# Performance work log

Measured on AMD Instinct MI355X. Metric: run time of the kernel, lower is better.

## Reference

```python
import jax, jax.numpy as jnp
import numpy as np

B_GRAPHS = 256
N_PER = 512
N = B_GRAPHS * N_PER            # 131072 nodes
E = 1048576                     # edges (avg degree 8)
H = 64                          # hidden_dim
L = 3                           # num_layers
R = 128                         # rnn_dim
NODE_IN = 2
EDGE_IN = 2
OUT = 2
JK = L * H


def setup_inputs() -> dict:
    key = jax.random.key(0)
    ks = jax.random.split(key, 40)
    # intra-graph random edges
    g = jax.random.randint(ks[0], (E,), 0, B_GRAPHS)
    src = g * N_PER + jax.random.randint(ks[1], (E,), 0, N_PER)
    dst = g * N_PER + jax.random.randint(ks[2], (E,), 0, N_PER)
    edge_index = jnp.stack([src, dst]).astype(jnp.int64)
    batch = jnp.repeat(jnp.arange(B_GRAPHS, dtype=jnp.int64), N_PER)

    p = lambda k, shp: jax.random.normal(k, shp, jnp.float32) * 0.1
    return dict(
        x=jax.random.normal(ks[3], (N, NODE_IN), jnp.float32),
        edge_attr=jax.random.normal(ks[4], (E, EDGE_IN), jnp.float32),
        node_W=p(ks[5], (NODE_IN, H)), node_b=p(ks[6], (H,)),
        edgeemb_W=p(ks[7], (EDGE_IN, H)), edgeemb_b=p(ks[8], (H,)),
        gat_W=p(ks[9], (L, H, H)), gat_Wedge=p(ks[10], (L, H, H)),
        gat_att_src=p(ks[11], (L, H)), gat_att_dst=p(ks[12], (L, H)),
        gat_att_edge=p(ks[13], (L, H)), gat_b=p(ks[14], (L, H)),
        gru_wih_f=p(ks[15], (3 * R, JK)), gru_whh_f=p(ks[16], (3 * R, R)),
        gru_bih_f=p(ks[17], (3 * R,)), gru_bhh_f=p(ks[18], (3 * R,)),
        gru_wih_b=p(ks[19], (3 * R, JK)), gru_whh_b=p(ks[20], (3 * R, R)),
        gru_bih_b=p(ks[21], (3 * R,)), gru_bhh_b=p(ks[22], (3 * R,)),
        head_W1=p(ks[23], (2 * R, 64)), head_b1=p(ks[24], (64,)),
        head_W2=p(ks[25], (64, OUT)), head_b2=p(ks[26], (OUT,)),
        edge_index=edge_index, batch=batch,
    )


def _gru_dir(xs, wih, whh, bih, bhh):
    # xs: [T, B, F] -> outputs [T, B, R]  (PyTorch GRU cell equations)
    gx = xs @ wih.T + bih  # precompute input gates [T, B, 3R]
    h0 = jnp.zeros((xs.shape[1], R), xs.dtype)

    def step(h, g):
        gh = h @ whh.T + bhh
        r = jax.nn.sigmoid(g[..., :R] + gh[..., :R])
        z = jax.nn.sigmoid(g[..., R:2 * R] + gh[..., R:2 * R])
        n = jnp.tanh(g[..., 2 * R:] + r * gh[..., 2 * R:])
        hn = (1.0 - z) * n + z * h
        return hn, hn

    _, ys = jax.lax.scan(step, h0, gx)
    return ys


def _forward(x, edge_attr, node_W, node_b, edgeemb_W, edgeemb_b,
             gat_W, gat_Wedge, gat_att_src, gat_att_dst, gat_att_edge, gat_b,
             gru_wih_f, gru_whh_f, gru_bih_f, gru_bhh_f,
             gru_wih_b, gru_whh_b, gru_bih_b, gru_bhh_b,
             head_W1, head_b1, head_W2, head_b2, edge_index, batch):
    src, dst = edge_index[0], edge_index[1]
    h = x @ node_W + node_b                     # [N, H]
    e = edge_attr @ edgeemb_W + edgeemb_b       # [E, H]

    # PyG GATConv default add_self_loops=True, fill_value='mean':
    # self-loop edge feature = mean of incoming edge features per node
    ones = jnp.ones((E,), e.dtype)
    deg = jax.ops.segment_sum(ones, dst, num_segments=N)
    e_loop = jax.ops.segment_sum(e, dst, num_segments=N) / jnp.maximum(deg, 1.0)[:, None]
    ar = jnp.arange(N, dtype=src.dtype)
    srcF = jnp.concatenate([src, ar])
    dstF = jnp.concatenate([dst, ar])
    eF = jnp.concatenate([e, e_loop], axis=0)   # [E+N, H]

    outs = []
    for l in range(L):
        xp = h @ gat_W[l]                                   # [N, H]
        a_s = xp @ gat_att_src[l]                           # [N]
        a_d = xp @ gat_att_dst[l]                           # [N]
        a_e = (eF @ gat_Wedge[l]) @ gat_att_edge[l]         # [E+N]
        alpha = jax.nn.leaky_relu(a_s[srcF] + a_d[dstF] + a_e, 0.2)
        m = jax.ops.segment_max(alpha, dstF, num_segments=N)
        ex = jnp.exp(alpha - m[dstF])
        den = jax.ops.segment_sum(ex, dstF, num_segments=N)
        w = ex / den[dstF]                                  # segment softmax
        agg = jax.ops.segment_sum(w[:, None] * xp[srcF], dstF, num_segments=N) + gat_b[l]
        h = jax.nn.leaky_relu(agg, 0.01)                    # F.leaky_relu default slope
        outs.append(h)

    h_jk = jnp.concatenate(outs, axis=-1)                   # [N, JK]
    # to_dense_batch: sorted equal-size graphs -> dense reshape, mask all True
    dense = h_jk.reshape(B_GRAPHS, N_PER, JK)
    xs = dense.transpose(1, 0, 2)                           # [T, B, JK]
    yf = _gru_dir(xs, gru_wih_f, gru_whh_f, gru_bih_f, gru_bhh_f)
    yb = _gru_dir(xs[::-1], gru_wih_b, gru_whh_b, gru_bih_b, gru_bhh_b)[::-1]
    rnn_out = jnp.concatenate([yf, yb], axis=-1).transpose(1, 0, 2)  # [B, T, 2R]
    out = jax.nn.relu(rnn_out @ head_W1 + head_b1) @ head_W2 + head_b2
    return out.reshape(N, OUT)                              # out[mask], mask full


def reference(x, edge_attr, node_W, node_b, edgeemb_W, edgeemb_b,
              gat_W, gat_Wedge, gat_att_src, gat_att_dst, gat_att_edge, gat_b,
              gru_wih_f, gru_whh_f, gru_bih_f, gru_bhh_f,
              gru_wih_b, gru_whh_b, gru_bih_b, gru_bhh_b,
              head_W1, head_b1, head_W2, head_b2, edge_index, batch):
    return _forward(x, edge_attr, node_W, node_b, edgeemb_W, edgeemb_b,
                    gat_W, gat_Wedge, gat_att_src, gat_att_dst, gat_att_edge, gat_b,
                    gru_wih_f, gru_whh_f, gru_bih_f, gru_bhh_f,
                    gru_wih_b, gru_whh_b, gru_bih_b, gru_bhh_b,
                    head_W1, head_b1, head_W2, head_b2, edge_index, batch)
```

## Files before the change

### kernel.cpp

```cpp
#include <hip/hip_runtime.h>
#include <cstdint>
#include <cstddef>

typedef _Float16 half_t;
typedef _Float16 half8 __attribute__((ext_vector_type(8)));
typedef float f32x4 __attribute__((ext_vector_type(4)));

constexpr int NN = 131072;
constexpr int NE = 1048576;
constexpr int NPER = 512;

#define DEVINL __device__ __forceinline__

DEVINL float sigm_(float x){ float e = __expf(-x); return __builtin_amdgcn_rcpf(1.f+e); }
DEVINL float tanh_(float x){
  x = fminf(15.f, fmaxf(-15.f, x));
  float e = __expf(-2.f*x);
  return (1.f-e)*__builtin_amdgcn_rcpf(1.f+e);
}

#define LDS_BARRIER() asm volatile("s_waitcnt lgkmcnt(0)\ns_barrier" ::: "memory")


__global__ void const_kernel(const float* __restrict__ gatWe,
                             const float* __restrict__ attE, const float* __restrict__ eW,
                             const float* __restrict__ eb, float* __restrict__ cc){
  int l = blockIdx.x, k = threadIdx.x;
  const float* Wel = gatWe + l*4096;
  float s3=0.f;
  for (int j=0;j<64;j++) s3 += Wel[k*64+j]*attE[l*64+j];
  float c0 = eW[k]*s3, c1 = eW[64+k]*s3, cb = eb[k]*s3;
  for (int off=1; off<64; off<<=1){
    c0 += __shfl_xor(c0,off); c1 += __shfl_xor(c1,off); cb += __shfl_xor(cb,off);
  }
  if (k==0){ cc[l]=c0; cc[3+l]=c1; cc[6+l]=cb; }
}

__global__ void prep_pack(const float* __restrict__ wih_f, const float* __restrict__ wih_b,
                          const float* __restrict__ head_W1, const float* __restrict__ gat_W,
                          const float* __restrict__ bih_f, const float* __restrict__ bih_b,
                          const float* __restrict__ whh_f, const float* __restrict__ whh_b,
                          half_t* __restrict__ BcombT, half_t* __restrict__ W1T,
                          half_t* __restrict__ BTgat, float* __restrict__ bias_comb,
                          half_t* __restrict__ whh16){
  int gid = blockIdx.x*256 + threadIdx.x;
  if (gid < 147456){
    int j = gid/192, k = gid%192;
    float v = (j<384)? wih_f[j*192+k] : wih_b[(j-384)*192+k];
    BcombT[gid] = (half_t)v;
  } else if (gid < 163840){
    int i = gid - 147456;
    int n = i>>8, k = i&255;
    W1T[i] = (half_t)head_W1[k*64+n];
  } else if (gid < 176128){
    int i = gid - 163840;
    int l = i>>12, r = i&4095;
    int n = r>>6, k = r&63;
    BTgat[i] = (half_t)gat_W[l*4096 + k*64 + n];
  } else if (gid < 176896){
    int i = gid - 176128;
    int j = (i<384)? i : i-384;
    bias_comb[i] = (i<384)? bih_f[j] : bih_b[j];
  } else if (gid < 275200){
    int i = gid - 176896;
    float v = (i<49152)? whh_f[i] : whh_b[i-49152];
    whh16[i] = (half_t)v;
  }
}

__global__ void bias_fold(const float* __restrict__ bhh_f, const float* __restrict__ bhh_b,
                          float* __restrict__ bias_comb){
  int i = threadIdx.x + blockIdx.x*256;
  if (i < 256)      bias_comb[i]       += bhh_f[i];
  else if (i < 512) bias_comb[i+128]   += bhh_b[i-256];
}

__global__ __launch_bounds__(256) void embed_kernel(const float* __restrict__ x,
                            const float* __restrict__ nW, const float* __restrict__ nb,
                            half_t* __restrict__ h){
  int gid = blockIdx.x*256 + threadIdx.x;
  int n = gid>>6, j = gid&63;
  float v = x[2*n]*nW[j] + x[2*n+1]*nW[64+j] + nb[j];
  h[(size_t)n*64+j] = (half_t)v;
}

__global__ __launch_bounds__(256) void deg_count(const int* __restrict__ ei,
                          int* __restrict__ deg, int* __restrict__ tmp){
  int e = blockIdx.x*256 + threadIdx.x;
  int dt = ei[NE+e];
  tmp[e] = atomicAdd(&deg[dt],1);
}

__global__ __launch_bounds__(256) void scan1(const int* __restrict__ deg, int* __restrict__ rowstart,
                      int* __restrict__ bsum){
  __shared__ int sc[256];
  int b=blockIdx.x, t=threadIdx.x, i=b*256+t;
  int v=deg[i]; sc[t]=v; __syncthreads();
  for (int off=1; off<256; off<<=1){
    int tv = (t>=off)? sc[t-off] : 0;
    __syncthreads(); sc[t]+=tv; __syncthreads();
  }
  rowstart[i]=sc[t]-v;
  if (t==255) bsum[b]=sc[255];
}
__global__ void scan2(int* __restrict__ bsum){
  __shared__ int sc[512];
  int t=threadIdx.x; int v=bsum[t]; sc[t]=v; __syncthreads();
  for (int off=1; off<512; off<<=1){
    int tv = (t>=off)? sc[t-off] : 0;
    __syncthreads(); sc[t]+=tv; __syncthreads();
  }
  bsum[t]=sc[t]-v;
}
__global__ __launch_bounds__(256) void scan3(int* __restrict__ rowstart, const int* __restrict__ bsum){
  int b=blockIdx.x, t=threadIdx.x, i=b*256+t;
  rowstart[i]+=bsum[b];
}

__global__ __launch_bounds__(256) void fill2(const int* __restrict__ ei, const float* __restrict__ ea,
                      const int* __restrict__ rowstart, const int* __restrict__ tmp,
                      int4* __restrict__ rec){
  int e = blockIdx.x*256 + threadIdx.x;
  int dt = ei[NE+e];
  int slot = rowstart[dt] + tmp[e];
  int4 r;
  r.x = ei[e];
  r.y = __float_as_int(ea[2*e]);
  r.z = __float_as_int(ea[2*e+1]);
  r.w = dt;
  rec[slot] = r;
}

__global__ __launch_bounds__(256) void means_kernel(const int* __restrict__ deg, const int* __restrict__ rowstart,
                         const int4* __restrict__ rec, float2* __restrict__ m01){
  int n = blockIdx.x*256 + threadIdx.x;
  int st = rowstart[n], cnt = deg[n];
  float s0=0.f, s1=0.f;
  for (int i=0;i<cnt;i++){
    int4 r = rec[st+i];
    s0 += __int_as_float(r.y);
    s1 += __int_as_float(r.z);
  }
  float inv = 1.f/(float)max(cnt,1);
  float2 m; m.x = s0*inv; m.y = s1*inv;
  m01[n] = m;
}

__global__ __launch_bounds__(256) void gemm_xp(const half_t* __restrict__ A, int lda,
                        const half_t* __restrict__ BT,
                        const float* __restrict__ attS, const float* __restrict__ attD,
                        half_t* __restrict__ xp, float* __restrict__ a_s, float* __restrict__ a_d){
  __shared__ half_t As[128*32];
  __shared__ half_t Bs[64*32];
  const int tid = threadIdx.x, m0 = blockIdx.x*128;
  const int w = tid>>6, lane = tid&63;
  const int lm = lane&15, quad = lane>>4;
  const int wm0 = w*32;
  f32x4 acc[2][4] = {};
  for (int k0=0;k0<64;k0+=32){
    {
      const int c0 = tid*2;
      #pragma unroll
      for (int u=0;u<2;u++){
        int c=c0+u; int row=c>>2; int off=(c&3)*8;
        *(half8*)(&As[row*32+off]) = *(const half8*)(&A[(size_t)(m0+row)*lda + k0 + off]);
      }
      int c=tid; int row=c>>2; int off=(c&3)*8;
      *(half8*)(&Bs[row*32+off]) = *(const half8*)(&BT[(size_t)row*64 + k0 + off]);
    }
    __syncthreads();
    half8 af[2], bf[4];
    #pragma unroll
    for (int nt=0;nt<4;nt++) bf[nt] = *(const half8*)(&Bs[(nt*16+lm)*32 + quad*8]);
    #pragma unroll
    for (int mt=0;mt<2;mt++) af[mt] = *(const half8*)(&As[(wm0+mt*16+lm)*32 + quad*8]);
    #pragma unroll
    for (int mt=0;mt<2;mt++)
      #pragma unroll
      for (int nt=0;nt<4;nt++)
        acc[mt][nt] = __builtin_amdgcn_mfma_f32_16x16x32_f16(af[mt], bf[nt], acc[mt][nt], 0,0,0);
    __syncthreads();
  }
  float vsv[4], vdv[4];
  #pragma unroll
  for (int nt=0;nt<4;nt++){ vsv[nt]=attS[nt*16+lm]; vdv[nt]=attD[nt*16+lm]; }
  #pragma unroll
  for (int mt=0;mt<2;mt++)
   #pragma unroll
   for (int r=0;r<4;r++){
    int m = m0+wm0+mt*16+quad*4+r;
    float ps=0.f, pd=0.f;
    #pragma unroll
    for (int nt=0;nt<4;nt++){
      float v = acc[mt][nt][r];
      xp[(size_t)m*64 + nt*16+lm] = (half_t)v;
      ps += v*vsv[nt]; pd += v*vdv[nt];
    }
    ps += __shfl_xor(ps,1); ps += __shfl_xor(ps,2); ps += __shfl_xor(ps,4); ps += __shfl_xor(ps,8);
    pd += __shfl_xor(pd,1); pd += __shfl_xor(pd,2); pd += __shfl_xor(pd,4); pd += __shfl_xor(pd,8);
    if (lm==0){ a_s[m]=ps; a_d[m]=pd; }
  }
}

__global__ __launch_bounds__(256) void edge_w(const int4* __restrict__ rec,
                       const float* __restrict__ a_s, const float* __restrict__ a_d,
                       const float* __restrict__ cc, int l, int2* __restrict__ sw,
                       const int* __restrict__ deg, const float2* __restrict__ m01,
                       float* __restrict__ wsf){
  int b = blockIdx.x;
  if (b < 4096){
    int s = b*256 + threadIdx.x;
    int4 r = rec[s];
    float al = a_s[r.x] + a_d[r.w]
             + __int_as_float(r.y)*cc[l] + __int_as_float(r.z)*cc[3+l] + cc[6+l];
    al = al>0.f? al : 0.2f*al;
    int2 o;
    o.x = (r.x & 511) | ((r.w & 127) << 16);
    o.y = __float_as_int(__expf(al));
    sw[s] = o;
  } else {
    int n = (b-4096)*256 + threadIdx.x;
    int cnt = deg[n];
    float2 m = m01[n];
    float ael = cnt? (m.x*cc[l] + m.y*cc[3+l] + cc[6+l]) : 0.f;
    float asl = a_s[n] + a_d[n] + ael;
    asl = asl>0.f? asl : 0.2f*asl;
    wsf[n] = __expf(asl);
  }
}

constexpr int SWCAP = 1536;
__global__ __launch_bounds__(512,4) void agg_lds(const int* __restrict__ rowstart, const int* __restrict__ deg,
                          const int2* __restrict__ sw, const float* __restrict__ wsf, int l,
                          const half_t* __restrict__ xp, const float* __restrict__ bias,
                          half_t* __restrict__ hjk){
  __shared__ int2  swl[SWCAP];
  __shared__ float nwsf[128];
  __shared__ int   ncnt[128];
  const int tid = threadIdx.x;
  const int nbase = blockIdx.x*128;
  const half_t* __restrict__ xpg = xp + ((size_t)(nbase >> 9))*32768;
  const int segst = rowstart[nbase];
  const int segend = rowstart[nbase+127] + deg[nbase+127];
  const int segcnt = segend - segst;
  const int w = tid>>6, lane = tid&63;
  int scap = segcnt < SWCAP ? segcnt : SWCAP;
  for (int i=tid; i<scap; i+=512) swl[i] = sw[segst+i];
  if (tid < 128){
    nwsf[tid] = wsf[nbase + tid];
    ncnt[tid] = deg[nbase + tid];
  }
  const int e0 = rowstart[nbase + w*16] - segst;
  const int e1 = (w==7) ? segcnt : (rowstart[nbase + w*16 + 16] - segst);
  __syncthreads();
  const float bv = bias[lane];
  const int nlb = nbase & 511;

  auto flush = [&](int cur, float acc, float den){
    float wv = nwsf[cur];
    float xs = (float)xpg[(size_t)(nlb + cur)*64 + lane];
    float v = (acc + wv*xs)/(den + wv) + bv;
    v = v>0.f? v : 0.01f*v;
    hjk[(size_t)(nbase + cur)*192 + l*64 + lane] = (half_t)v;
  };

  if (segcnt <= SWCAP){
    const int cnt = e1 - e0;
    if (cnt > 0){
      int2  P[8];
      float X[8];
      #pragma unroll
      for (int i=0;i<8;i++){
        int idx = e0 + (i < cnt ? i : cnt-1);
        P[i] = swl[idx];
        X[i] = (float)xpg[(size_t)(P[i].x & 511)*64 + lane];
      }
      int cur = P[0].x >> 16;
      float acc = 0.f, den = 0.f;
      int e = e0;
      for (; e + 8 <= e1; e += 8){
        #pragma unroll
        for (int i=0;i<8;i++){
          int dl = P[i].x >> 16;
          if (dl != cur){ flush(cur, acc, den); cur = dl; acc = 0.f; den = 0.f; }
          float ww = __int_as_float(P[i].y);
          acc += ww*X[i]; den += ww;
          int nidx = e + 8 + i;
          int cidx = nidx < e1 ? nidx : e1-1;
          P[i] = swl[cidx];
          X[i] = (float)xpg[(size_t)(P[i].x & 511)*64 + lane];
        }
      }
      int rem = e1 - e;
      #pragma unroll
      for (int i=0;i<8;i++){
        if (i < rem){
          int dl = P[i].x >> 16;
          if (dl != cur){ flush(cur, acc, den); cur = dl; acc = 0.f; den = 0.f; }
          float ww = __int_as_float(P[i].y);
          acc += ww*X[i]; den += ww;
        }
      }
      flush(cur, acc, den);
    }
    #pragma unroll
    for (int i=0;i<16;i++){
      int li = w*16+i;
      if (ncnt[li]==0) flush(li, 0.f, 0.f);
    }
  } else {
    if (e0 < e1){
      int2 p = sw[segst+e0];
      float xv = (float)xpg[(size_t)(p.x & 511)*64 + lane];
      int cur = p.x >> 16;
      float acc = 0.f, den = 0.f;
      for (int e = e0; e < e1; ++e){
        int en = (e+1 < e1) ? e+1 : e;
        int2 pn = sw[segst+en];
        float xvn = (float)xpg[(size_t)(pn.x & 511)*64 + lane];
        int dl = p.x >> 16;
        if (dl != cur){
          flush(cur, acc, den);
          cur = dl; acc = 0.f; den = 0.f;
        }
        float ww = __int_as_float(p.y);
        acc += ww*xv; den += ww;
        p = pn; xv = xvn;
      }
      flush(cur, acc, den);
    }
    #pragma unroll
    for (int i=0;i<16;i++){
      int li = w*16+i;
      if (ncnt[li]==0) flush(li, 0.f, 0.f);
    }
  }
}

__global__ __launch_bounds__(256) void gemm_head(const half_t* __restrict__ A,
                        const half_t* __restrict__ W1T, const float* __restrict__ b1,
                        const float* __restrict__ W2, const float* __restrict__ b2,
                        float* __restrict__ out){
  __shared__ half_t As[128*32];
  __shared__ half_t Bs[64*32];
  const int tid = threadIdx.x, m0 = blockIdx.x*128;
  const int w = tid>>6, lane = tid&63;
  const int lm = lane&15, quad = lane>>4;
  const int wm0 = w*32;
  f32x4 acc[2][4] = {};
  for (int k0=0;k0<256;k0+=32){
    {
      const int c0 = tid*2;
      #pragma unroll
      for (int u=0;u<2;u++){
        int c=c0+u; int row=c>>2; int off=(c&3)*8;
        *(half8*)(&As[row*32+off]) = *(const half8*)(&A[(size_t)(m0+row)*256 + k0 + off]);
      }
      int c=tid; int row=c>>2; int off=(c&3)*8;
      *(half8*)(&Bs[row*32+off]) = *(const half8*)(&W1T[(size_t)row*256 + k0 + off]);
    }
    __syncthreads();
    half8 af[2], bf[4];
    #pragma unroll
    for (int nt=0;nt<4;nt++) bf[nt] = *(const half8*)(&Bs[(nt*16+lm)*32 + quad*8]);
    #pragma unroll
    for (int mt=0;mt<2;mt++) af[mt] = *(const half8*)(&As[(wm0+mt*16+lm)*32 + quad*8]);
    #pragma unroll
    for (int mt=0;mt<2;mt++)
      #pragma unroll
      for (int nt=0;nt<4;nt++)
        acc[mt][nt] = __builtin_amdgcn_mfma_f32_16x16x32_f16(af[mt], bf[nt], acc[mt][nt], 0,0,0);
    __syncthreads();
  }
  float b1v[4], w20[4], w21[4];
  #pragma unroll
  for (int nt=0;nt<4;nt++){
    int n = nt*16+lm;
    b1v[nt]=b1[n]; w20[nt]=W2[n*2]; w21[nt]=W2[n*2+1];
  }
  float b20=b2[0], b21=b2[1];
  #pragma unroll
  for (int mt=0;mt<2;mt++)
   #pragma unroll
   for (int r=0;r<4;r++){
    int m = m0+wm0+mt*16+quad*4+r;
    float p0=0.f, p1=0.f;
    #pragma unroll
    for (int nt=0;nt<4;nt++){
      float v = acc[mt][nt][r] + b1v[nt];
      v = v>0.f? v : 0.f;
      p0 += v*w20[nt]; p1 += v*w21[nt];
    }
    p0 += __shfl_xor(p0,1); p0 += __shfl_xor(p0,2); p0 += __shfl_xor(p0,4); p0 += __shfl_xor(p0,8);
    p1 += __shfl_xor(p1,1); p1 += __shfl_xor(p1,2); p1 += __shfl_xor(p1,4); p1 += __shfl_xor(p1,8);
    if (lm==0){
      out[(size_t)m*2]   = p0 + b20;
      out[(size_t)m*2+1] = p1 + b21;
    }
  }
}

__global__ __launch_bounds__(512,1) void gru_fused(
    const half_t* __restrict__ whh16, const float* __restrict__ bhh_f, const float* __restrict__ bhh_b,
    const half_t* __restrict__ gxf, const half_t* __restrict__ gxb,
    float* __restrict__ hstate, half_t* __restrict__ y, int c, int gruBlocks,
    const half_t* __restrict__ hjk, const half_t* __restrict__ BcombT, const float* __restrict__ biasc,
    half_t* __restrict__ gxf_n, half_t* __restrict__ gxb_n, int s0f, int s0b){
  __shared__ __align__(16) char SMEM[16384];
  const int bid = blockIdx.x;
  const int tid = threadIdx.x;
  if (bid < gruBlocks){
    __builtin_amdgcn_s_setprio(1);
    auto& H = *(half_t (*)[2][16][132])SMEM;

    const int d = bid >> 6, gblk = bid & 63;
    const half_t* __restrict__ gx = d ? gxb : gxf;
    const float* bhh = d ? bhh_b : bhh_f;
    const int w = tid >> 6, lane = tid & 63;
    const int l15 = lane & 15, quad = lane >> 4;
    const int unit = w*16 + l15;

    half8 bf[3][4];
    float bhn = bhh[256 + unit];
    {
      const half_t* wbase = whh16 + (size_t)d*49152;
      #pragma unroll
      for (int g=0; g<3; g++){
        const half_t* wp = wbase + (size_t)(g*128 + unit)*128;
        #pragma unroll
        for (int kk=0; kk<4; kk++)
          bf[g][kk] = *(const half8*)(wp + kk*32 + quad*8);
      }
    }

    float hreg = hstate[((size_t)d*256 + gblk*4 + quad)*128 + unit];

    const int jstep = d ? -384 : 384;
    const int ystep = d ? -256 : 256;
    const int j0 = d ? 127 : 0;
    const int pos0 = d ? (511 - c*128) : (c*128);

    const int cgg = tid >> 6;
    const int cpart = (tid & 63)*2;
    half_t* yptr = y + ((size_t)(gblk*4 + cgg)*512 + pos0)*256 + d*128 + cpart;

    long gofs = ((long)(gblk*4 + quad)*128 + j0)*384 + unit;
    half_t gA0,gA1,gA2, gB0,gB1,gB2;
    gA0 = gx[gofs]; gA1 = gx[gofs+128]; gA2 = gx[gofs+256]; gofs += jstep;
    gB0 = gx[gofs]; gB1 = gx[gofs+128]; gB2 = gx[gofs+256]; gofs += jstep;

    H[0][quad*4][unit] = (half_t)hreg;
    LDS_BARRIER();

    auto stepf = [&](int rd, int wr2, half_t& c0, half_t& c1, half_t& c2,
                     bool cp, bool pf){
      if (cp && tid < 256){
        uint hv = *(const uint*)&H[rd][cgg*4][cpart];
        *(uint*)yptr = hv;
        yptr += ystep;
      }
      half8 af[4] = {};
      if ((l15 & 3) == 0){
        #pragma unroll
        for (int kk=0; kk<4; kk++)
          af[kk] = *(const half8*)&H[rd][l15][kk*32 + quad*8];
      }
      f32x4 Pa[3] = {}, Pb[3] = {};
      #pragma unroll
      for (int g=0; g<3; g++){
        Pa[g] = __builtin_amdgcn_mfma_f32_16x16x32_f16(af[0], bf[g][0], Pa[g], 0,0,0);
        Pb[g] = __builtin_amdgcn_mfma_f32_16x16x32_f16(af[2], bf[g][2], Pb[g], 0,0,0);
        Pa[g] = __builtin_amdgcn_mfma_f32_16x16x32_f16(af[1], bf[g][1], Pa[g], 0,0,0);
        Pb[g] = __builtin_amdgcn_mfma_f32_16x16x32_f16(af[3], bf[g][3], Pb[g], 0,0,0);
      }
      float p0 = Pa[0][0] + Pb[0][0];
      float p1 = Pa[1][0] + Pb[1][0];
      float p2 = Pa[2][0] + Pb[2][0];
      float rr = sigm_((float)c0 + p0);
      float zz = sigm_((float)c1 + p1);
      float nn = tanh_((float)c2 + rr*(p2 + bhn));
      float hn = nn + zz*(hreg - nn);
      hreg = hn;
      H[wr2][quad*4][unit] = (half_t)hn;
      if (pf){
        c0 = gx[gofs]; c1 = gx[gofs+128]; c2 = gx[gofs+256];
        gofs += jstep;
      }
      LDS_BARRIER();
    };

    stepf(0,1, gA0,gA1,gA2, false, true);
    stepf(1,0, gB0,gB1,gB2, true,  true);
    for (int it=1; it<63; it++){
      stepf(0,1, gA0,gA1,gA2, true, true);
      stepf(1,0, gB0,gB1,gB2, true, true);
    }
    stepf(0,1, gA0,gA1,gA2, true, false);
    stepf(1,0, gB0,gB1,gB2, true, false);
    if (tid < 256){
      uint hv = *(const uint*)&H[0][cgg*4][cpart];
      *(uint*)yptr = hv;
    }
    __builtin_amdgcn_s_setprio(0);
    hstate[((size_t)d*256 + gblk*4 + quad)*128 + unit] = hreg;
  } else {
    half_t* As = (half_t*)SMEM;
    half_t* Bs = (half_t*)(SMEM + 8192);
    const int gb = bid - gruBlocks;
    const int bx = gb & 255, by = gb >> 8;
    const int m0 = bx*128;
    const bool back = by >= 3;
    const int n0 = (back ? by-3 : by)*128;
    const int step0 = back ? s0b : s0f;
    half_t* C = back ? gxb_n : gxf_n;
    const half_t* BTh = BcombT + (back ? (size_t)384*192 : 0);
    const float* bh = biasc + (back ? 384 : 0);
    const int w = tid>>6, lane = tid&63;
    const int lm = lane&15, quad = lane>>4;
    const int wm0 = (w>>2)*64, wn0 = (w&3)*32;
    f32x4 acc[4][2] = {};
    for (int k0=0; k0<192; k0+=32){
      {
        int cidx = tid; int row = cidx>>2; int off = (cidx&3)*8;
        int m = m0+row;
        size_t arow = (size_t)(m>>7)*512 + step0 + (m&127);
        *(half8*)(&As[row*32+off]) = *(const half8*)(&hjk[arow*192 + k0 + off]);
        *(half8*)(&Bs[row*32+off]) = *(const half8*)(&BTh[(size_t)(n0+row)*192 + k0 + off]);
      }
      __syncthreads();
      half8 af[4], bfr[2];
      #pragma unroll
      for (int nt=0;nt<2;nt++) bfr[nt] = *(const half8*)(&Bs[(wn0+nt*16+lm)*32 + quad*8]);
      #pragma unroll
      for (int mt=0;mt<4;mt++) af[mt] = *(const half8*)(&As[(wm0+mt*16+lm)*32 + quad*8]);
      #pragma unroll
      for (int mt=0;mt<4;mt++)
        #pragma unroll
        for (int nt=0;nt<2;nt++)
          acc[mt][nt] = __builtin_amdgcn_mfma_f32_16x16x32_f16(af[mt], bfr[nt], acc[mt][nt], 0,0,0);
      __syncthreads();
    }
    #pragma unroll
    for (int mt=0;mt<4;mt++)
     #pragma unroll
     for (int nt=0;nt<2;nt++)
      #pragma unroll
      for (int r=0;r<4;r++){
        int m = m0+wm0+mt*16+quad*4+r;
        int n = n0+wn0+nt*16+lm;
        float v = acc[mt][nt][r] + bh[n];
        C[(size_t)m*384 + n] = (half_t)v;
      }
  }
}

extern "C" void kernel_launch(void* const* d_in, const int* in_sizes, int n_in,
                              void* d_out, int out_size, void* d_ws, size_t ws_size,
                              hipStream_t stream) {
  const float* x       = (const float*)d_in[0];
  const float* ea      = (const float*)d_in[1];
  const float* node_W  = (const float*)d_in[2];
  const float* node_b  = (const float*)d_in[3];
  const float* eW      = (const float*)d_in[4];
  const float* eb      = (const float*)d_in[5];
  const float* gat_W   = (const float*)d_in[6];
  const float* gat_We  = (const float*)d_in[7];
  const float* attS    = (const float*)d_in[8];
  const float* attD    = (const float*)d_in[9];
  const float* attE    = (const float*)d_in[10];
  const float* gat_b   = (const float*)d_in[11];
  const float* wih_f   = (const float*)d_in[12];
  const float* whh_f   = (const float*)d_in[13];
  const float* bih_f   = (const float*)d_in[14];
  const float* bhh_f   = (const float*)d_in[15];
  const float* wih_b   = (const float*)d_in[16];
  const float* whh_b   = (const float*)d_in[17];
  const float* bih_b   = (const float*)d_in[18];
  const float* bhh_b   = (const float*)d_in[19];
  const float* head_W1 = (const float*)d_in[20];
  const float* head_b1 = (const float*)d_in[21];
  const float* head_W2 = (const float*)d_in[22];
  const float* head_b2 = (const float*)d_in[23];
  const int*   ei      = (const int*)d_in[24];
  float* out = (float*)d_out;
  char* ws = (char*)d_ws;
  (void)in_sizes; (void)n_in; (void)out_size; (void)ws_size;

  size_t o = 0;
  auto alloc = [&](size_t bytes)->size_t{ size_t r=o; o += (bytes+255)&~(size_t)255; return r; };
  size_t o_cc     = alloc(16*4);
  size_t o_biasc  = alloc(768*4);
  size_t o_BcombT = alloc((size_t)768*192*2);
  size_t o_BTgat  = alloc((size_t)3*4096*2);
  size_t o_W1T    = alloc((size_t)64*256*2);
  size_t o_whh16  = alloc((size_t)2*49152*2);
  size_t o_hstate = alloc((size_t)2*256*128*4);
  size_t shared_base = o;

  size_t o_deg    = alloc((size_t)NN*4);
  size_t zero_end = o;
  size_t o_tmp    = alloc((size_t)NE*4);
  size_t o_rows   = alloc((size_t)NN*4);
  size_t o_bsum   = alloc(512*4);
  size_t o_rec    = alloc((size_t)NE*16);
  size_t o_sw     = alloc((size_t)NE*8);
  size_t o_m01    = alloc((size_t)NN*8);
  size_t o_as     = alloc((size_t)NN*4);
  size_t o_ad     = alloc((size_t)NN*4);
  size_t o_wsf    = alloc((size_t)NN*4);
  size_t o_h      = alloc((size_t)NN*64*2);
  size_t o_xp     = alloc((size_t)NN*64*2);
  size_t gat_end  = o;
  size_t gat_size = gat_end - shared_base;

  const size_t GXC    = (size_t)256*128*384*2;
  const size_t HJK_SZ = (size_t)NN*192*2;
  size_t shared_sz = gat_size > 4*GXC ? gat_size : 4*GXC;
  size_t o_gx0f = shared_base;
  size_t o_gx0b = shared_base + GXC;
  size_t o_gx1f = shared_base + 2*GXC;
  size_t o_gx1b = shared_base + 3*GXC;
  size_t o_hjk = shared_base + shared_sz;
  size_t o_y   = o_hjk + HJK_SZ;

  int*    deg    = (int*)(ws+o_deg);
  int*    tmp    = (int*)(ws+o_tmp);
  int*    rows   = (int*)(ws+o_rows);
  int*    bsum   = (int*)(ws+o_bsum);
  int4*   rec    = (int4*)(ws+o_rec);
  int2*   sw     = (int2*)(ws+o_sw);
  float2* m01    = (float2*)(ws+o_m01);
  float*  a_s    = (float*)(ws+o_as);
  float*  a_d    = (float*)(ws+o_ad);
  float*  wsf    = (float*)(ws+o_wsf);
  float*  cc     = (float*)(ws+o_cc);
  float*  biasc  = (float*)(ws+o_biasc);
  half_t* h      = (half_t*)(ws+o_h);
  half_t* xp     = (half_t*)(ws+o_xp);
  half_t* hjk    = (half_t*)(ws+o_hjk);
  half_t* BcombT = (half_t*)(ws+o_BcombT);
  half_t* BTgat  = (half_t*)(ws+o_BTgat);
  half_t* W1T    = (half_t*)(ws+o_W1T);
  half_t* whh16  = (half_t*)(ws+o_whh16);
  float*  hstate = (float*)(ws+o_hstate);
  half_t* gxbuf[2][2] = {{(half_t*)(ws+o_gx0f), (half_t*)(ws+o_gx0b)},
                         {(half_t*)(ws+o_gx1f), (half_t*)(ws+o_gx1b)}};
  half_t* y      = (half_t*)(ws+o_y);

  hipMemsetAsync(ws+shared_base, 0, zero_end-shared_base, stream);
  hipMemsetAsync(ws+o_hstate, 0, (size_t)2*256*128*4, stream);

  const_kernel<<<3,64,0,stream>>>(gat_We, attE, eW, eb, cc);
  prep_pack<<<1075,256,0,stream>>>(wih_f, wih_b, head_W1, gat_W, bih_f, bih_b, whh_f, whh_b,
                                   BcombT, W1T, BTgat, biasc, whh16);
  bias_fold<<<2,256,0,stream>>>(bhh_f, bhh_b, biasc);
  embed_kernel<<<32768,256,0,stream>>>(x, node_W, node_b, h);
  deg_count<<<4096,256,0,stream>>>(ei, deg, tmp);
  scan1<<<512,256,0,stream>>>(deg, rows, bsum);
  scan2<<<1,512,0,stream>>>(bsum);
  scan3<<<512,256,0,stream>>>(rows, bsum);
  fill2<<<4096,256,0,stream>>>(ei, ea, rows, tmp, rec);
  means_kernel<<<512,256,0,stream>>>(deg, rows, rec, m01);

  for (int l=0;l<3;l++){
    const half_t* in = (l==0)? h : (hjk + (size_t)(l-1)*64);
    int lda = (l==0)? 64 : 192;
    gemm_xp<<<1024,256,0,stream>>>(in, lda, BTgat + (size_t)l*4096, attS + l*64, attD + l*64, xp, a_s, a_d);
    edge_w<<<4608,256,0,stream>>>(rec, a_s, a_d, cc, l, sw, deg, m01, wsf);
    agg_lds<<<1024,512,0,stream>>>(rows, deg, sw, wsf, l, xp, gat_b + l*64, hjk);
  }

  gru_fused<<<1536,512,0,stream>>>(whh16, bhh_f, bhh_b, gxbuf[0][0], gxbuf[0][1], hstate, y, 0, 0,
                                   hjk, BcombT, biasc, gxbuf[0][0], gxbuf[0][1], 0, 384);
  for (int c=0;c<4;c++){
    int buf = c&1, nbuf = (c+1)&1;
    int grid = 128 + (c<3 ? 1536 : 0);
    gru_fused<<<grid,512,0,stream>>>(whh16, bhh_f, bhh_b, gxbuf[buf][0], gxbuf[buf][1], hstate, y, c, 128,
                                     hjk, BcombT, biasc, gxbuf[nbuf][0], gxbuf[nbuf][1],
                                     (c+1)*128, (2-c)*128);
  }

  gemm_head<<<1024,256,0,stream>>>(y, W1T, head_b1, head_W2, head_b2, out);
}
```

Before: 709.3 us.

## Split GRU block into compute waves handling two units and copy-out waves

The GRU recurrence block now uses only waves 0-3 for the MFMA and gate math, each thread handling two hidden units (unit and unit+64). Waves 4-7 only copy the previous hidden state from LDS to the output y. This takes the global store traffic off the compute waves' critical path, but doubles the per-thread MFMA chain and register use on the compute waves, which can lengthen each serial step.

```diff
diff --git a/kernel.cpp b/kernel.cpp
--- a/kernel.cpp
+++ b/kernel.cpp
@@ -418,91 +418,122 @@
     const float* bhh = d ? bhh_b : bhh_f;
     const int w = tid >> 6, lane = tid & 63;
     const int l15 = lane & 15, quad = lane >> 4;
-    const int unit = w*16 + l15;
-
-    half8 bf[3][4];
-    float bhn = bhh[256 + unit];
-    {
-      const half_t* wbase = whh16 + (size_t)d*49152;
-      #pragma unroll
-      for (int g=0; g<3; g++){
-        const half_t* wp = wbase + (size_t)(g*128 + unit)*128;
-        #pragma unroll
-        for (int kk=0; kk<4; kk++)
-          bf[g][kk] = *(const half8*)(wp + kk*32 + quad*8);
-      }
-    }
-
-    float hreg = hstate[((size_t)d*256 + gblk*4 + quad)*128 + unit];
+    const bool cw = (w < 4);
+    const int unit = (w & 3)*16 + l15;
 
     const int jstep = d ? -384 : 384;
     const int ystep = d ? -256 : 256;
     const int j0 = d ? 127 : 0;
     const int pos0 = d ? (511 - c*128) : (c*128);
 
-    const int cgg = tid >> 6;
-    const int cpart = (tid & 63)*2;
+    const int tid2 = tid & 255;
+    const int cgg = tid2 >> 6;
+    const int cpart = (tid2 & 63)*2;
     half_t* yptr = y + ((size_t)(gblk*4 + cgg)*512 + pos0)*256 + d*128 + cpart;
 
-    long gofs = ((long)(gblk*4 + quad)*128 + j0)*384 + unit;
-    half_t gA0,gA1,gA2, gB0,gB1,gB2;
-    gA0 = gx[gofs]; gA1 = gx[gofs+128]; gA2 = gx[gofs+256]; gofs += jstep;
-    gB0 = gx[gofs]; gB1 = gx[gofs+128]; gB2 = gx[gofs+256]; gofs += jstep;
-
-    H[0][quad*4][unit] = (half_t)hreg;
+    half8 bf1[3][4], bf2[3][4];
+    float bhn1 = 0.f, bhn2 = 0.f, hreg1 = 0.f, hreg2 = 0.f;
+    long gofs = 0;
+    half_t A0,A1,A2,A3,A4,A5, B0,B1,B2,B3,B4,B5;
+    A0=A1=A2=A3=A4=A5=B0=B1=B2=B3=B4=B5=(half_t)0.f;
+    if (cw){
+      bhn1 = bhh[256 + unit];
+      bhn2 = bhh[256 + unit + 64];
+      const half_t* wbase = whh16 + (size_t)d*49152;
+      #pragma unroll
+      for (int g=0; g<3; g++){
+        const half_t* wp1 = wbase + (size_t)(g*128 + unit)*128;
+        const half_t* wp2 = wbase + (size_t)(g*128 + unit + 64)*128;
+        #pragma unroll
+        for (int kk=0; kk<4; kk++){
+          bf1[g][kk] = *(const half8*)(wp1 + kk*32 + quad*8);
+          bf2[g][kk] = *(const half8*)(wp2 + kk*32 + quad*8);
+        }
+      }
+      hreg1 = hstate[((size_t)d*256 + gblk*4 + quad)*128 + unit];
+      hreg2 = hstate[((size_t)d*256 + gblk*4 + quad)*128 + unit + 64];
+      gofs = ((long)(gblk*4 + quad)*128 + j0)*384 + unit;
+      A0 = gx[gofs]; A1 = gx[gofs+128]; A2 = gx[gofs+256];
+      A3 = gx[gofs+64]; A4 = gx[gofs+192]; A5 = gx[gofs+320]; gofs += jstep;
+      B0 = gx[gofs]; B1 = gx[gofs+128]; B2 = gx[gofs+256];
+      B3 = gx[gofs+64]; B4 = gx[gofs+192]; B5 = gx[gofs+320]; gofs += jstep;
+      H[0][quad*4][unit]      = (half_t)hreg1;
+      H[0][quad*4][unit + 64] = (half_t)hreg2;
+    }
     LDS_BARRIER();
 
-    auto stepf = [&](int rd, int wr2, half_t& c0, half_t& c1, half_t& c2,
+    auto stepf = [&](int rd, int wr2,
+                     half_t& c0, half_t& c1, half_t& c2,
+                     half_t& c3, half_t& c4, half_t& c5,
                      bool cp, bool pf){
-      if (cp && tid < 256){
-        uint hv = *(const uint*)&H[rd][cgg*4][cpart];
-        *(uint*)yptr = hv;
-        yptr += ystep;
-      }
-      half8 af[4] = {};
-      if ((l15 & 3) == 0){
+      if (cw){
+        half8 af[4] = {};
+        if ((l15 & 3) == 0){
+          #pragma unroll
+          for (int kk=0; kk<4; kk++)
+            af[kk] = *(const half8*)&H[rd][l15][kk*32 + quad*8];
+        }
+        f32x4 Pa[3] = {}, Pb[3] = {}, Qa[3] = {}, Qb[3] = {};
         #pragma unroll
-        for (int kk=0; kk<4; kk++)
-          af[kk] = *(const half8*)&H[rd][l15][kk*32 + quad*8];
-      }
-      f32x4 Pa[3] = {}, Pb[3] = {};
-      #pragma unroll
-      for (int g=0; g<3; g++){
-        Pa[g] = __builtin_amdgcn_mfma_f32_16x16x32_f16(af[0], bf[g][0], Pa[g], 0,0,0);
-        Pb[g] = __builtin_amdgcn_mfma_f32_16x16x32_f16(af[2], bf[g][2], Pb[g], 0,0,0);
-        Pa[g] = __builtin_amdgcn_mfma_f32_16x16x32_f16(af[1], bf[g][1], Pa[g], 0,0,0);
-        Pb[g] = __builtin_amdgcn_mfma_f32_16x16x32_f16(af[3], bf[g][3], Pb[g], 0,0,0);
-      }
-      float p0 = Pa[0][0] + Pb[0][0];
-      float p1 = Pa[1][0] + Pb[1][0];
-      float p2 = Pa[2][0] + Pb[2][0];
-      float rr = sigm_((float)c0 + p0);
-      float zz = sigm_((float)c1 + p1);
-      float nn = tanh_((float)c2 + rr*(p2 + bhn));
-      float hn = nn + zz*(hreg - nn);
-      hreg = hn;
-      H[wr2][quad*4][unit] = (half_t)hn;
-      if (pf){
-        c0 = gx[gofs]; c1 = gx[gofs+128]; c2 = gx[gofs+256];
-        gofs += jstep;
+        for (int g=0; g<3; g++){
+          Pa[g] = __builtin_amdgcn_mfma_f32_16x16x32_f16(af[0], bf1[g][0], Pa[g], 0,0,0);
+          Qa[g] = __builtin_amdgcn_mfma_f32_16x16x32_f16(af[0], bf2[g][0], Qa[g], 0,0,0);
+          Pb[g] = __builtin_amdgcn_mfma_f32_16x16x32_f16(af[2], bf1[g][2], Pb[g], 0,0,0);
+          Qb[g] = __builtin_amdgcn_mfma_f32_16x16x32_f16(af[2], bf2[g][2], Qb[g], 0,0,0);
+          Pa[g] = __builtin_amdgcn_mfma_f32_16x16x32_f16(af[1], bf1[g][1], Pa[g], 0,0,0);
+          Qa[g] = __builtin_amdgcn_mfma_f32_16x16x32_f16(af[1], bf2[g][1], Qa[g], 0,0,0);
+          Pb[g] = __builtin_amdgcn_mfma_f32_16x16x32_f16(af[3], bf1[g][3], Pb[g], 0,0,0);
+          Qb[g] = __builtin_amdgcn_mfma_f32_16x16x32_f16(af[3], bf2[g][3], Qb[g], 0,0,0);
+        }
+        float p0 = Pa[0][0] + Pb[0][0];
+        float p1 = Pa[1][0] + Pb[1][0];
+        float p2 = Pa[2][0] + Pb[2][0];
+        float q0 = Qa[0][0] + Qb[0][0];
+        float q1 = Qa[1][0] + Qb[1][0];
+        float q2 = Qa[2][0] + Qb[2][0];
+        float rr1 = sigm_((float)c0 + p0);
+        float rr2 = sigm_((float)c3 + q0);
+        float zz1 = sigm_((float)c1 + p1);
+        float zz2 = sigm_((float)c4 + q1);
+        float nn1 = tanh_((float)c2 + rr1*(p2 + bhn1));
+        float nn2 = tanh_((float)c5 + rr2*(q2 + bhn2));
+        float hn1 = nn1 + zz1*(hreg1 - nn1);
+        float hn2 = nn2 + zz2*(hreg2 - nn2);
+        hreg1 = hn1; hreg2 = hn2;
+        H[wr2][quad*4][unit]      = (half_t)hn1;
+        H[wr2][quad*4][unit + 64] = (half_t)hn2;
+        if (pf){
+          c0 = gx[gofs]; c1 = gx[gofs+128]; c2 = gx[gofs+256];
+          c3 = gx[gofs+64]; c4 = gx[gofs+192]; c5 = gx[gofs+320];
+          gofs += jstep;
+        }
+      } else {
+        if (cp){
+          uint hv = *(const uint*)&H[rd][cgg*4][cpart];
+          *(uint*)yptr = hv;
+          yptr += ystep;
+        }
       }
       LDS_BARRIER();
     };
 
-    stepf(0,1, gA0,gA1,gA2, false, true);
-    stepf(1,0, gB0,gB1,gB2, true,  true);
+    stepf(0,1, A0,A1,A2,A3,A4,A5, false, true);
+    stepf(1,0, B0,B1,B2,B3,B4,B5, true,  true);
     for (int it=1; it<63; it++){
-      stepf(0,1, gA0,gA1,gA2, true, true);
-      stepf(1,0, gB0,gB1,gB2, true, true);
-    }
-    stepf(0,1, gA0,gA1,gA2, true, false);
-    stepf(1,0, gB0,gB1,gB2, true, false);
-    if (tid < 256){
+      stepf(0,1, A0,A1,A2,A3,A4,A5, true, true);
+      stepf(1,0, B0,B1,B2,B3,B4,B5, true, true);
+    }
+    stepf(0,1, A0,A1,A2,A3,A4,A5, true, false);
+    stepf(1,0, B0,B1,B2,B3,B4,B5, true, false);
+    if (!cw){
       uint hv = *(const uint*)&H[0][cgg*4][cpart];
       *(uint*)yptr = hv;
     }
     __builtin_amdgcn_s_setprio(0);
-    hstate[((size_t)d*256 + gblk*4 + quad)*128 + unit] = hreg;
+    if (cw){
+      hstate[((size_t)d*256 + gblk*4 + quad)*128 + unit]      = hreg1;
+      hstate[((size_t)d*256 + gblk*4 + quad)*128 + unit + 64] = hreg2;
+    }
   } else {
     half_t* As = (half_t*)SMEM;
     half_t* Bs = (half_t*)(SMEM + 8192);
```

Result: no change. 715.8 us (+0.9%).

## Split fused GRU/gate-GEMM kernel into separate serialized launches

Applied to the files above, without the earlier changes.

The fused kernel that ran the recurrent GRU blocks alongside the next chunk's input-gate GEMM blocks is split into two kernels, gemm_gx and gru_run, launched one after the other on the same stream. This drops the overlap of the GEMM with the latency-bound recurrence and adds launches. The GRU also now writes each hidden value straight to y per step with scalar half stores, instead of a delayed coalesced 32-bit copy from LDS. The split lets each kernel have its own launch bounds and LDS footprint, but it serializes work that previously ran concurrently.

```diff
diff --git a/kernel.cpp b/kernel.cpp
--- a/kernel.cpp
+++ b/kernel.cpp
@@ -400,158 +400,148 @@
   }
 }
 
-__global__ __launch_bounds__(512,1) void gru_fused(
+__global__ __launch_bounds__(512) void gemm_gx(
+    const half_t* __restrict__ hjk, const half_t* __restrict__ BcombT,
+    const float* __restrict__ biasc,
+    half_t* __restrict__ gxf_n, half_t* __restrict__ gxb_n, int s0f, int s0b){
+  __shared__ half_t As[128*32];
+  __shared__ half_t Bs[128*32];
+  const int tid = threadIdx.x;
+  const int gb = blockIdx.x;
+  const int bx = gb & 255, by = gb >> 8;
+  const int m0 = bx*128;
+  const bool back = by >= 3;
+  const int n0 = (back ? by-3 : by)*128;
+  const int step0 = back ? s0b : s0f;
+  half_t* C = back ? gxb_n : gxf_n;
+  const half_t* BTh = BcombT + (back ? (size_t)384*192 : 0);
+  const float* bh = biasc + (back ? 384 : 0);
+  const int w = tid>>6, lane = tid&63;
+  const int lm = lane&15, quad = lane>>4;
+  const int wm0 = (w>>2)*64, wn0 = (w&3)*32;
+  f32x4 acc[4][2] = {};
+  for (int k0=0; k0<192; k0+=32){
+    {
+      int cidx = tid; int row = cidx>>2; int off = (cidx&3)*8;
+      int m = m0+row;
+      size_t arow = (size_t)(m>>7)*512 + step0 + (m&127);
+      *(half8*)(&As[row*32+off]) = *(const half8*)(&hjk[arow*192 + k0 + off]);
+      *(half8*)(&Bs[row*32+off]) = *(const half8*)(&BTh[(size_t)(n0+row)*192 + k0 + off]);
+    }
+    __syncthreads();
+    half8 af[4], bfr[2];
+    #pragma unroll
+    for (int nt=0;nt<2;nt++) bfr[nt] = *(const half8*)(&Bs[(wn0+nt*16+lm)*32 + quad*8]);
+    #pragma unroll
+    for (int mt=0;mt<4;mt++) af[mt] = *(const half8*)(&As[(wm0+mt*16+lm)*32 + quad*8]);
+    #pragma unroll
+    for (int mt=0;mt<4;mt++)
+      #pragma unroll
+      for (int nt=0;nt<2;nt++)
+        acc[mt][nt] = __builtin_amdgcn_mfma_f32_16x16x32_f16(af[mt], bfr[nt], acc[mt][nt], 0,0,0);
+    __syncthreads();
+  }
+  #pragma unroll
+  for (int mt=0;mt<4;mt++)
+   #pragma unroll
+   for (int nt=0;nt<2;nt++)
+    #pragma unroll
+    for (int r=0;r<4;r++){
+      int m = m0+wm0+mt*16+quad*4+r;
+      int n = n0+wn0+nt*16+lm;
+      float v = acc[mt][nt][r] + bh[n];
+      C[(size_t)m*384 + n] = (half_t)v;
+    }
+}
+
+__global__ __launch_bounds__(512,1) void gru_run(
     const half_t* __restrict__ whh16, const float* __restrict__ bhh_f, const float* __restrict__ bhh_b,
     const half_t* __restrict__ gxf, const half_t* __restrict__ gxb,
-    float* __restrict__ hstate, half_t* __restrict__ y, int c, int gruBlocks,
-    const half_t* __restrict__ hjk, const half_t* __restrict__ BcombT, const float* __restrict__ biasc,
-    half_t* __restrict__ gxf_n, half_t* __restrict__ gxb_n, int s0f, int s0b){
-  __shared__ __align__(16) char SMEM[16384];
+    float* __restrict__ hstate, half_t* __restrict__ y, int c){
+  __shared__ half_t H[2][16][132];
   const int bid = blockIdx.x;
   const int tid = threadIdx.x;
-  if (bid < gruBlocks){
-    __builtin_amdgcn_s_setprio(1);
-    auto& H = *(half_t (*)[2][16][132])SMEM;
-
-    const int d = bid >> 6, gblk = bid & 63;
-    const half_t* __restrict__ gx = d ? gxb : gxf;
-    const float* bhh = d ? bhh_b : bhh_f;
-    const int w = tid >> 6, lane = tid & 63;
-    const int l15 = lane & 15, quad = lane >> 4;
-    const int unit = w*16 + l15;
-
-    half8 bf[3][4];
-    float bhn = bhh[256 + unit];
-    {
-      const half_t* wbase = whh16 + (size_t)d*49152;
-      #pragma unroll
-      for (int g=0; g<3; g++){
-        const half_t* wp = wbase + (size_t)(g*128 + unit)*128;
-        #pragma unroll
-        for (int kk=0; kk<4; kk++)
-          bf[g][kk] = *(const half8*)(wp + kk*32 + quad*8);
-      }
-    }
-
-    float hreg = hstate[((size_t)d*256 + gblk*4 + quad)*128 + unit];
-
-    const int jstep = d ? -384 : 384;
-    const int ystep = d ? -256 : 256;
-    const int j0 = d ? 127 : 0;
-    const int pos0 = d ? (511 - c*128) : (c*128);
-
-    const int cgg = tid >> 6;
-    const int cpart = (tid & 63)*2;
-    half_t* yptr = y + ((size_t)(gblk*4 + cgg)*512 + pos0)*256 + d*128 + cpart;
-
-    long gofs = ((long)(gblk*4 + quad)*128 + j0)*384 + unit;
-    half_t gA0,gA1,gA2, gB0,gB1,gB2;
-    gA0 = gx[gofs]; gA1 = gx[gofs+128]; gA2 = gx[gofs+256]; gofs += jstep;
-    gB0 = gx[gofs]; gB1 = gx[gofs+128]; gB2 = gx[gofs+256]; gofs += jstep;
-
-    H[0][quad*4][unit] = (half_t)hreg;
+  __builtin_amdgcn_s_setprio(1);
+  const int d = bid >> 6, gblk = bid & 63;
+  const half_t* __restrict__ gx = d ? gxb : gxf;
+  const float* bhh = d ? bhh_b : bhh_f;
+  const int w = tid >> 6, lane = tid & 63;
+  const int l15 = lane & 15, quad = lane >> 4;
+  const int unit = w*16 + l15;
+
+  half8 bf[3][4];
+  float bhn = bhh[256 + unit];
+  {
+    const half_t* wbase = whh16 + (size_t)d*49152;
+    #pragma unroll
+    for (int g=0; g<3; g++){
+      const half_t* wp = wbase + (size_t)(g*128 + unit)*128;
+      #pragma unroll
+      for (int kk=0; kk<4; kk++)
+        bf[g][kk] = *(const half8*)(wp + kk*32 + quad*8);
+    }
+  }
+
+  float hreg = hstate[((size_t)d*256 + gblk*4 + quad)*128 + unit];
+
+  const int jstep = d ? -384 : 384;
+  const int j0 = d ? 127 : 0;
+  const int pos0 = d ? (511 - c*128) : (c*128);
+  const long ystep = d ? -256 : 256;
+  half_t* yptr = y + ((size_t)(gblk*4 + quad)*512 + pos0)*256 + d*128 + unit;
+
+  long gofs = ((long)(gblk*4 + quad)*128 + j0)*384 + unit;
+  half_t A0,A1,A2, B0,B1,B2;
+  A0 = gx[gofs]; A1 = gx[gofs+128]; A2 = gx[gofs+256]; gofs += jstep;
+  B0 = gx[gofs]; B1 = gx[gofs+128]; B2 = gx[gofs+256]; gofs += jstep;
+
+  H[0][quad*4][unit] = (half_t)hreg;
+  LDS_BARRIER();
+
+  auto stepf = [&](int rd, int wr2, half_t& c0, half_t& c1, half_t& c2, bool pf){
+    half8 af[4] = {};
+    if ((l15 & 3) == 0){
+      #pragma unroll
+      for (int kk=0; kk<4; kk++)
+        af[kk] = *(const half8*)&H[rd][l15][kk*32 + quad*8];
+    }
+    f32x4 Pa[3] = {}, Pb[3] = {};
+    #pragma unroll
+    for (int g=0; g<3; g++){
+      Pa[g] = __builtin_amdgcn_mfma_f32_16x16x32_f16(af[0], bf[g][0], Pa[g], 0,0,0);
+      Pb[g] = __builtin_amdgcn_mfma_f32_16x16x32_f16(af[2], bf[g][2], Pb[g], 0,0,0);
+      Pa[g] = __builtin_amdgcn_mfma_f32_16x16x32_f16(af[1], bf[g][1], Pa[g], 0,0,0);
+      Pb[g] = __builtin_amdgcn_mfma_f32_16x16x32_f16(af[3], bf[g][3], Pb[g], 0,0,0);
+    }
+    float p0 = Pa[0][0] + Pb[0][0];
+    float p1 = Pa[1][0] + Pb[1][0];
+    float p2 = Pa[2][0] + Pb[2][0];
+    float rr = sigm_((float)c0 + p0);
+    float zz = sigm_((float)c1 + p1);
+    float nn = tanh_((float)c2 + rr*(p2 + bhn));
+    float hn = nn + zz*(hreg - nn);
+    hreg = hn;
+    half_t hh = (half_t)hn;
+    H[wr2][quad*4][unit] = hh;
+    *yptr = hh;
+    yptr += ystep;
+    if (pf){
+      c0 = gx[gofs]; c1 = gx[gofs+128]; c2 = gx[gofs+256];
+      gofs += jstep;
+    }
     LDS_BARRIER();
-
-    auto stepf = [&](int rd, int wr2, half_t& c0, half_t& c1, half_t& c2,
-                     bool cp, bool pf){
-      if (cp && tid < 256){
-        uint hv = *(const uint*)&H[rd][cgg*4][cpart];
-        *(uint*)yptr = hv;
-        yptr += ystep;
-      }
-      half8 af[4] = {};
-      if ((l15 & 3) == 0){
-        #pragma unroll
-        for (int kk=0; kk<4; kk++)
-          af[kk] = *(const half8*)&H[rd][l15][kk*32 + quad*8];
-      }
-      f32x4 Pa[3] = {}, Pb[3] = {};
-      #pragma unroll
-      for (int g=0; g<3; g++){
-        Pa[g] = __builtin_amdgcn_mfma_f32_16x16x32_f16(af[0], bf[g][0], Pa[g], 0,0,0);
-        Pb[g] = __builtin_amdgcn_mfma_f32_16x16x32_f16(af[2], bf[g][2], Pb[g], 0,0,0);
-        Pa[g] = __builtin_amdgcn_mfma_f32_16x16x32_f16(af[1], bf[g][1], Pa[g], 0,0,0);
-        Pb[g] = __builtin_amdgcn_mfma_f32_16x16x32_f16(af[3], bf[g][3], Pb[g], 0,0,0);
-      }
-      float p0 = Pa[0][0] + Pb[0][0];
-      float p1 = Pa[1][0] + Pb[1][0];
-      float p2 = Pa[2][0] + Pb[2][0];
-      float rr = sigm_((float)c0 + p0);
-      float zz = sigm_((float)c1 + p1);
-      float nn = tanh_((float)c2 + rr*(p2 + bhn));
-      float hn = nn + zz*(hreg - nn);
-      hreg = hn;
-      H[wr2][quad*4][unit] = (half_t)hn;
-      if (pf){
-        c0 = gx[gofs]; c1 = gx[gofs+128]; c2 = gx[gofs+256];
-        gofs += jstep;
-      }
-      LDS_BARRIER();
-    };
-
-    stepf(0,1, gA0,gA1,gA2, false, true);
-    stepf(1,0, gB0,gB1,gB2, true,  true);
-    for (int it=1; it<63; it++){
-      stepf(0,1, gA0,gA1,gA2, true, true);
-      stepf(1,0, gB0,gB1,gB2, true, true);
-    }
-    stepf(0,1, gA0,gA1,gA2, true, false);
-    stepf(1,0, gB0,gB1,gB2, true, false);
-    if (tid < 256){
-      uint hv = *(const uint*)&H[0][cgg*4][cpart];
-      *(uint*)yptr = hv;
-    }
-    __builtin_amdgcn_s_setprio(0);
-    hstate[((size_t)d*256 + gblk*4 + quad)*128 + unit] = hreg;
-  } else {
-    half_t* As = (half_t*)SMEM;
-    half_t* Bs = (half_t*)(SMEM + 8192);
-    const int gb = bid - gruBlocks;
-    const int bx = gb & 255, by = gb >> 8;
-    const int m0 = bx*128;
-    const bool back = by >= 3;
-    const int n0 = (back ? by-3 : by)*128;
-    const int step0 = back ? s0b : s0f;
-    half_t* C = back ? gxb_n : gxf_n;
-    const half_t* BTh = BcombT + (back ? (size_t)384*192 : 0);
-    const float* bh = biasc + (back ? 384 : 0);
-    const int w = tid>>6, lane = tid&63;
-    const int lm = lane&15, quad = lane>>4;
-    const int wm0 = (w>>2)*64, wn0 = (w&3)*32;
-    f32x4 acc[4][2] = {};
-    for (int k0=0; k0<192; k0+=32){
-      {
-        int cidx = tid; int row = cidx>>2; int off = (cidx&3)*8;
-        int m = m0+row;
-        size_t arow = (size_t)(m>>7)*512 + step0 + (m&127);
-        *(half8*)(&As[row*32+off]) = *(const half8*)(&hjk[arow*192 + k0 + off]);
-        *(half8*)(&Bs[row*32+off]) = *(const half8*)(&BTh[(size_t)(n0+row)*192 + k0 + off]);
-      }
-      __syncthreads();
-      half8 af[4], bfr[2];
-      #pragma unroll
-      for (int nt=0;nt<2;nt++) bfr[nt] = *(const half8*)(&Bs[(wn0+nt*16+lm)*32 + quad*8]);
-      #pragma unroll
-      for (int mt=0;mt<4;mt++) af[mt] = *(const half8*)(&As[(wm0+mt*16+lm)*32 + quad*8]);
-      #pragma unroll
-      for (int mt=0;mt<4;mt++)
-        #pragma unroll
-        for (int nt=0;nt<2;nt++)
-          acc[mt][nt] = __builtin_amdgcn_mfma_f32_16x16x32_f16(af[mt], bfr[nt], acc[mt][nt], 0,0,0);
-      __syncthreads();
-    }
-    #pragma unroll
-    for (int mt=0;mt<4;mt++)
-     #pragma unroll
-     for (int nt=0;nt<2;nt++)
-      #pragma unroll
-      for (int r=0;r<4;r++){
-        int m = m0+wm0+mt*16+quad*4+r;
-        int n = n0+wn0+nt*16+lm;
-        float v = acc[mt][nt][r] + bh[n];
-        C[(size_t)m*384 + n] = (half_t)v;
-      }
-  }
+  };
+
+  stepf(0,1, A0,A1,A2, true);
+  stepf(1,0, B0,B1,B2, true);
+  for (int it=1; it<63; it++){
+    stepf(0,1, A0,A1,A2, true);
+    stepf(1,0, B0,B1,B2, true);
+  }
+  stepf(0,1, A0,A1,A2, false);
+  stepf(1,0, B0,B1,B2, false);
+  __builtin_amdgcn_s_setprio(0);
+  hstate[((size_t)d*256 + gblk*4 + quad)*128 + unit] = hreg;
 }
 
 extern "C" void kernel_launch(void* const* d_in, const int* in_sizes, int n_in,
@@ -670,14 +660,13 @@
     agg_lds<<<1024,512,0,stream>>>(rows, deg, sw, wsf, l, xp, gat_b + l*64, hjk);
   }
 
-  gru_fused<<<1536,512,0,stream>>>(whh16, bhh_f, bhh_b, gxbuf[0][0], gxbuf[0][1], hstate, y, 0, 0,
-                                   hjk, BcombT, biasc, gxbuf[0][0], gxbuf[0][1], 0, 384);
+  gemm_gx<<<1536,512,0,stream>>>(hjk, BcombT, biasc, gxbuf[0][0], gxbuf[0][1], 0, 384);
   for (int c=0;c<4;c++){
     int buf = c&1, nbuf = (c+1)&1;
-    int grid = 128 + (c<3 ? 1536 : 0);
-    gru_fused<<<grid,512,0,stream>>>(whh16, bhh_f, bhh_b, gxbuf[buf][0], gxbuf[buf][1], hstate, y, c, 128,
-                                     hjk, BcombT, biasc, gxbuf[nbuf][0], gxbuf[nbuf][1],
+    if (c<3)
+      gemm_gx<<<1536,512,0,stream>>>(hjk, BcombT, biasc, gxbuf[nbuf][0], gxbuf[nbuf][1],
                                      (c+1)*128, (2-c)*128);
+    gru_run<<<128,512,0,stream>>>(whh16, bhh_f, bhh_b, gxbuf[buf][0], gxbuf[buf][1], hstate, y, c);
   }
 
   gemm_head<<<1024,256,0,stream>>>(y, W1T, head_b1, head_W2, head_b2, out);
```

Result: slower. 764.3 us (+7.8%).
